# Kernel optimization log

Hardware: AMD Instinct MI355X
Metric: run time of the kernel (lower is better)

Reference implementation:

```python
import jax, jax.numpy as jnp
import numpy as np

LN_EPS = 1e-5

def silu(x):
    return x * jax.nn.sigmoid(x)

def setup_inputs() -> dict:
    key = jax.random.key(0)
    ks = jax.random.split(key, 24)
    B, D = 131072, 256
    def w(k, shape, fan_in):
        return jax.random.uniform(k, shape, jnp.float32, -1.0, 1.0) / np.sqrt(fan_in)
    inp = {
        'x': jax.random.normal(ks[0], (B, D), jnp.float32),
        # stem: Linear(D,128) -> LN(128) -> SiLU -> Linear(128,64) -> SiLU
        'stem_w1': w(ks[1], (D, 128), D), 'stem_b1': w(ks[2], (128,), D),
        'ln_g': jnp.ones((128,), jnp.float32), 'ln_b': jnp.zeros((128,), jnp.float32),
        'stem_w2': w(ks[3], (128, 64), 128), 'stem_b2': w(ks[4], (64,), 128),
        # 4 experts: Linear(64,128)->SiLU->Linear(128,64)->SiLU, stacked on axis 0
        'ew1': w(ks[5], (4, 64, 128), 64), 'eb1': w(ks[6], (4, 128), 64),
        'ew2': w(ks[7], (4, 128, 64), 128), 'eb2': w(ks[8], (4, 64), 128),
        # gate: Linear(64,32)->SiLU->Linear(32,4)
        'gw1': w(ks[9], (64, 32), 64), 'gb1': w(ks[10], (32,), 64),
        'gw2': w(ks[11], (32, 4), 32), 'gb2': w(ks[12], (4,), 32),
        # shared: Linear(64,64)->SiLU
        'sw': w(ks[13], (64, 64), 64), 'sb': w(ks[14], (64,), 64),
        # 3 heads (strain, tensile, yield) stacked: Linear(64,32)->SiLU->Linear(32,1)
        'hw1': w(ks[15], (3, 64, 32), 64), 'hb1': w(ks[16], (3, 32), 64),
        'hw2': w(ks[17], (3, 32, 1), 32), 'hb2': w(ks[18], (3, 1), 32),
    }
    return inp

def reference(x, stem_w1, stem_b1, ln_g, ln_b, stem_w2, stem_b2,
              ew1, eb1, ew2, eb2, gw1, gb1, gw2, gb2, sw, sb,
              hw1, hb1, hw2, hb2):
    # stem (dropout = identity, eval mode)
    h = x @ stem_w1 + stem_b1                      # [B,128]
    mu = jnp.mean(h, -1, keepdims=True)
    var = jnp.mean(jnp.square(h - mu), -1, keepdims=True)
    h = (h - mu) * jax.lax.rsqrt(var + LN_EPS) * ln_g + ln_b
    h = silu(h)
    h = silu(h @ stem_w2 + stem_b2)                # [B,64]
    # gate
    g = silu(h @ gw1 + gb1)
    gate_w = jax.nn.softmax(g @ gw2 + gb2, axis=-1)  # [B,4]
    # experts: [B,64] x [4,64,128] -> [B,4,128]
    e = silu(jnp.einsum('bd,edh->beh', h, ew1) + eb1)
    e = silu(jnp.einsum('beh,ehd->bed', e, ew2) + eb2)  # [B,4,64]
    moe_h = jnp.einsum('bed,be->bd', e, gate_w)    # [B,64]
    # shared trunk (dropout = identity)
    feat = silu(moe_h @ sw + sb)                   # [B,64]
    # 3 heads
    hh = silu(jnp.einsum('bd,kdh->bkh', feat, hw1) + hb1)  # [B,3,32]
    out = (jnp.einsum('bkh,kho->bko', hh, hw2) + hb2)[..., 0]  # [B,3]
    return out
```

## Files before the change

### kernel.cpp

```cpp
#include <hip/hip_runtime.h>

typedef _Float16 f16;
typedef f16   f16x4 __attribute__((ext_vector_type(4)));
typedef f16   f16x8 __attribute__((ext_vector_type(8)));
typedef float f32x4 __attribute__((ext_vector_type(4)));

#define MFMA16(a, b, c) __builtin_amdgcn_mfma_f32_16x16x32_f16((a), (b), (c), 0, 0, 0)

#define IMG_W1   0
#define IMG_W2   32768
#define IMG_GW1  40960
#define IMG_EW1  43008
#define IMG_EW2  75776
#define IMG_SW   108544
#define IMG_HW1  112640

__device__ __forceinline__ float silu_f(float v) {
    return v * __builtin_amdgcn_rcpf(1.0f + __expf(-v));
}

__device__ void conv_blk(const float* __restrict__ src, f16* __restrict__ dst,
                         int srcN, int k0, int n0, int KB, int NB, int tid, int nth) {
    for (int i = tid; i < KB * NB; i += nth) {
        const int kk = i / NB, nn = i - kk * NB;
        dst[nn * KB + (kk ^ ((nn & 7) << 3))] = (f16)src[(long)(k0 + kk) * srcN + n0 + nn];
    }
}

__global__ void prep_weights(const float* __restrict__ w1, const float* __restrict__ w2,
                             const float* __restrict__ gw1, const float* __restrict__ ew1,
                             const float* __restrict__ ew2, const float* __restrict__ sw,
                             const float* __restrict__ hw1, f16* __restrict__ ws) {
    const int tid = blockIdx.x * 256 + threadIdx.x;
    const int nth = gridDim.x * 256;
    for (int kh = 0; kh < 2; ++kh)
        for (int nh = 0; nh < 2; ++nh)
            conv_blk(w1, ws + IMG_W1 + (kh * 2 + nh) * 8192, 128, kh * 128, nh * 64, 128, 64, tid, nth);
    conv_blk(w2,  ws + IMG_W2,  64, 0, 0, 128, 64, tid, nth);
    conv_blk(gw1, ws + IMG_GW1, 32, 0, 0,  64, 32, tid, nth);
    for (int e = 0; e < 4; ++e)
        for (int h = 0; h < 2; ++h) {
            conv_blk(ew1 + e * 8192, ws + IMG_EW1 + (e * 2 + h) * 4096, 128, 0, h * 64, 64, 64, tid, nth);
            conv_blk(ew2 + e * 8192, ws + IMG_EW2 + (e * 2 + h) * 4096,  64, h * 64, 0, 64, 64, tid, nth);
        }
    conv_blk(sw, ws + IMG_SW, 64, 0, 0, 64, 64, tid, nth);
    for (int h = 0; h < 3; ++h)
        conv_blk(hw1 + h * 2048, ws + IMG_HW1 + h * 2048, 32, 0, 0, 64, 32, tid, nth);
}

#define GLL16(g, l) __builtin_amdgcn_global_load_lds(                        \
    (const __attribute__((address_space(1))) void*)(g),                     \
    (__attribute__((address_space(3))) void*)(l), 16, 0, 0)

template<int S_F16>
__device__ __forceinline__ void stage_img(const f16* __restrict__ g, f16* l,
                                          int wv, int lane) {
    constexpr int QB = (S_F16 * 2) / 4;
    constexpr int CALLS = QB / 1024;
    const char* gs = (const char*)g + wv * QB + lane * 16;
    char* ls = (char*)l + wv * QB;
    #pragma unroll
    for (int i = 0; i < CALLS; ++i)
        GLL16(gs + i * 1024, ls + i * 1024);
}

__device__ __forceinline__ int swz_key(int mode, int r) {
    if (mode == 0) return (r & 7) << 3;
    if (mode == 1) return (r & 15) << 3;
    return ((((r >> 2) & 3) << 1) | (r & 1)) << 3;
}

template<int MODE>
__device__ __forceinline__ f16x8 ld_frag(const f16* base, int stride, int row_base, int k0) {
    const int lane = threadIdx.x & 63;
    const int r = row_base + (lane & 15);
    const int k = k0 + ((lane >> 4) << 3);
    return *(const f16x8*)(base + r * stride + (k ^ swz_key(MODE, r)));
}

template<int MODE>
__device__ __forceinline__ void st_frag(f16* base, int stride, int row_base, int col_base, f32x4 v) {
    const int lane = threadIdx.x & 63;
    const int c = col_base + (lane & 15);
    #pragma unroll
    for (int g = 0; g < 4; ++g) {
        const int r = row_base + ((lane >> 4) << 2) + g;
        base[r * stride + (c ^ swz_key(MODE, r))] = (f16)v[g];
    }
}

__device__ __forceinline__ void stage_x(const float* __restrict__ xsrc, f16* XACT, int half) {
    const int t = threadIdx.x;
    #pragma unroll 8
    for (int i = 0; i < 16; ++i) {
        const int idx4 = t + i * 256;
        const int r  = idx4 >> 5;
        const int kc = (idx4 & 31) << 2;
        const float4 v = *(const float4*)(xsrc + (long)r * 256 + half * 128 + kc);
        f16x4 o; o[0] = (f16)v.x; o[1] = (f16)v.y; o[2] = (f16)v.z; o[3] = (f16)v.w;
        *(f16x4*)(XACT + r * 128 + (kc ^ ((r & 15) << 3))) = o;
    }
}

__device__ __forceinline__ f32x4 reduce16(f32x4 v) {
    #pragma unroll
    for (int m = 1; m <= 8; m <<= 1) {
        f32x4 o;
        #pragma unroll
        for (int i = 0; i < 4; ++i) o[i] = __shfl_xor(v[i], m, 64);
        v += o;
    }
    return v;
}

__global__ __launch_bounds__(256, 3)
void fused_net_mfma(const float* __restrict__ x,   const f16* __restrict__ wsp,
                    const float* __restrict__ b1,  const float* __restrict__ lng,
                    const float* __restrict__ lnb, const float* __restrict__ b2,
                    const float* __restrict__ eb1, const float* __restrict__ eb2,
                    const float* __restrict__ gb1, const float* __restrict__ gw2,
                    const float* __restrict__ gb2, const float* __restrict__ sb,
                    const float* __restrict__ hb1, const float* __restrict__ hw2,
                    const float* __restrict__ hb2, float* __restrict__ out)
{
    __shared__ __align__(16) f16 lds[26624];
    f16* XACT = lds;
    f16* ACT1 = lds;
    f16* ACT2 = lds + 8192;
    f16* W    = lds + 16384;
    f16* G    = lds + 24576;

    const int lane = threadIdx.x & 63;
    const int wv   = threadIdx.x >> 6;
    const int c    = lane & 15;
    const long blockRow = (long)blockIdx.x * 128;
    const int waveRow = wv * 32;
    const float* xblk = x + blockRow * 256;

    f32x4 acc[2][8];
    #pragma unroll
    for (int n = 0; n < 8; ++n) {
        const float bv = b1[n * 16 + c];
        f32x4 t = {bv, bv, bv, bv};
        acc[0][n] = t; acc[1][n] = t;
    }
    #pragma unroll
    for (int kh = 0; kh < 2; ++kh) {
        if (kh) __syncthreads();
        stage_x(xblk, XACT, kh);
        stage_img<8192>(wsp + IMG_W1 + kh * 16384, W, wv, lane);
        __syncthreads();
        f16x8 af[2][4];
        #pragma unroll
        for (int m = 0; m < 2; ++m)
            #pragma unroll
            for (int ks = 0; ks < 4; ++ks)
                af[m][ks] = ld_frag<1>(XACT, 128, waveRow + m * 16, ks * 32);
        #pragma unroll
        for (int ks = 0; ks < 4; ++ks)
            #pragma unroll
            for (int n = 0; n < 4; ++n) {
                const f16x8 b = ld_frag<0>(W, 128, n * 16, ks * 32);
                acc[0][n] = MFMA16(af[0][ks], b, acc[0][n]);
                acc[1][n] = MFMA16(af[1][ks], b, acc[1][n]);
            }
        __syncthreads();
        stage_img<8192>(wsp + IMG_W1 + kh * 16384 + 8192, W, wv, lane);
        __syncthreads();
        #pragma unroll
        for (int ks = 0; ks < 4; ++ks)
            #pragma unroll
            for (int n = 0; n < 4; ++n) {
                const f16x8 b = ld_frag<0>(W, 128, n * 16, ks * 32);
                acc[0][4 + n] = MFMA16(af[0][ks], b, acc[0][4 + n]);
                acc[1][4 + n] = MFMA16(af[1][ks], b, acc[1][4 + n]);
            }
    }

    f32x4 mu[2], rs[2];
    #pragma unroll
    for (int m = 0; m < 2; ++m) {
        f32x4 s = {0, 0, 0, 0}, q = {0, 0, 0, 0};
        #pragma unroll
        for (int n = 0; n < 8; ++n) { s += acc[m][n]; q += acc[m][n] * acc[m][n]; }
        s = reduce16(s); q = reduce16(q);
        mu[m] = s * 0.0078125f;
        #pragma unroll
        for (int g = 0; g < 4; ++g) {
            const float var = q[g] * 0.0078125f - mu[m][g] * mu[m][g];
            rs[m][g] = rsqrtf(var + 1e-5f);
        }
    }
    __syncthreads();
    stage_img<8192>(wsp + IMG_W2,  W, wv, lane);
    stage_img<2048>(wsp + IMG_GW1, G, wv, lane);
    __syncthreads();

    f32x4 a2[2][4];
    #pragma unroll
    for (int n = 0; n < 4; ++n) {
        const float bv = b2[n * 16 + c];
        f32x4 t = {bv, bv, bv, bv};
        a2[0][n] = t; a2[1][n] = t;
    }
    #pragma unroll
    for (int half = 0; half < 2; ++half) {
        #pragma unroll
        for (int m = 0; m < 2; ++m)
            #pragma unroll
            for (int n = 0; n < 4; ++n) {
                const int j = half * 64 + n * 16 + c;
                const float gg = lng[j], bb = lnb[j];
                f32x4 v;
                #pragma unroll
                for (int g = 0; g < 4; ++g)
                    v[g] = silu_f((acc[m][half * 4 + n][g] - mu[m][g]) * rs[m][g] * gg + bb);
                st_frag<2>(ACT1, 64, waveRow + m * 16, n * 16, v);
            }
        #pragma unroll
        for (int ks = 0; ks < 2; ++ks) {
            const f16x8 a0 = ld_frag<2>(ACT1, 64, waveRow,      ks * 32);
            const f16x8 a1 = ld_frag<2>(ACT1, 64, waveRow + 16, ks * 32);
            #pragma unroll
            for (int n = 0; n < 4; ++n) {
                const f16x8 b = ld_frag<0>(W, 128, n * 16, half * 64 + ks * 32);
                a2[0][n] = MFMA16(a0, b, a2[0][n]);
                a2[1][n] = MFMA16(a1, b, a2[1][n]);
            }
        }
    }
    #pragma unroll
    for (int m = 0; m < 2; ++m)
        #pragma unroll
        for (int n = 0; n < 4; ++n) {
            f32x4 v;
            #pragma unroll
            for (int g = 0; g < 4; ++g) v[g] = silu_f(a2[m][n][g]);
            st_frag<2>(ACT2, 64, waveRow + m * 16, n * 16, v);
        }

    f32x4 gwt[2][4];
    {
        f32x4 ag[2][2];
        #pragma unroll
        for (int n = 0; n < 2; ++n) {
            const float bv = gb1[n * 16 + c];
            f32x4 t = {bv, bv, bv, bv};
            ag[0][n] = t; ag[1][n] = t;
        }
        #pragma unroll
        for (int ks = 0; ks < 2; ++ks) {
            const f16x8 a0 = ld_frag<2>(ACT2, 64, waveRow,      ks * 32);
            const f16x8 a1 = ld_frag<2>(ACT2, 64, waveRow + 16, ks * 32);
            #pragma unroll
            for (int n = 0; n < 2; ++n) {
                const f16x8 b = ld_frag<0>(G, 64, n * 16, ks * 32);
                ag[0][n] = MFMA16(a0, b, ag[0][n]);
                ag[1][n] = MFMA16(a1, b, ag[1][n]);
            }
        }
        const f32x4 gb2v = *(const f32x4*)gb2;
        #pragma unroll
        for (int m = 0; m < 2; ++m) {
            f32x4 pg[4] = {{0,0,0,0},{0,0,0,0},{0,0,0,0},{0,0,0,0}};
            #pragma unroll
            for (int n = 0; n < 2; ++n) {
                const int j = n * 16 + c;
                const f32x4 w4 = *(const f32x4*)(gw2 + j * 4);
                #pragma unroll
                for (int g = 0; g < 4; ++g)
                    pg[g] += silu_f(ag[m][n][g]) * w4;
            }
            #pragma unroll
            for (int g = 0; g < 4; ++g) {
                f32x4 l = reduce16(pg[g]) + gb2v;
                const float mx = fmaxf(fmaxf(l[0], l[1]), fmaxf(l[2], l[3]));
                f32x4 ee;
                #pragma unroll
                for (int o = 0; o < 4; ++o) ee[o] = __expf(l[o] - mx);
                const float inv = __builtin_amdgcn_rcpf(ee[0] + ee[1] + ee[2] + ee[3]);
                gwt[m][g] = ee * inv;
            }
        }
    }

    f32x4 moe[2][4] = {{{0,0,0,0},{0,0,0,0},{0,0,0,0},{0,0,0,0}},
                       {{0,0,0,0},{0,0,0,0},{0,0,0,0},{0,0,0,0}}};
    #pragma unroll
    for (int e = 0; e < 4; ++e) {
        f32x4 a2acc[2][4];
        #pragma unroll
        for (int n = 0; n < 4; ++n) {
            const float bv = eb2[e * 64 + n * 16 + c];
            f32x4 t = {bv, bv, bv, bv};
            a2acc[0][n] = t; a2acc[1][n] = t;
        }
        #pragma unroll
        for (int mh = 0; mh < 2; ++mh) {
            __syncthreads();
            stage_img<4096>(wsp + IMG_EW1 + (e * 2 + mh) * 4096, W,        wv, lane);
            stage_img<4096>(wsp + IMG_EW2 + (e * 2 + mh) * 4096, W + 4096, wv, lane);
            __syncthreads();
            f32x4 a1acc[2][4];
            #pragma unroll
            for (int n = 0; n < 4; ++n) {
                const float bv = eb1[e * 128 + mh * 64 + n * 16 + c];
                f32x4 t = {bv, bv, bv, bv};
                a1acc[0][n] = t; a1acc[1][n] = t;
            }
            #pragma unroll
            for (int ks = 0; ks < 2; ++ks) {
                const f16x8 a0 = ld_frag<2>(ACT2, 64, waveRow,      ks * 32);
                const f16x8 a1 = ld_frag<2>(ACT2, 64, waveRow + 16, ks * 32);
                #pragma unroll
                for (int n = 0; n < 4; ++n) {
                    const f16x8 b = ld_frag<0>(W, 64, n * 16, ks * 32);
                    a1acc[0][n] = MFMA16(a0, b, a1acc[0][n]);
                    a1acc[1][n] = MFMA16(a1, b, a1acc[1][n]);
                }
            }
            #pragma unroll
            for (int m = 0; m < 2; ++m)
                #pragma unroll
                for (int n = 0; n < 4; ++n) {
                    f32x4 v;
                    #pragma unroll
                    for (int g = 0; g < 4; ++g) v[g] = silu_f(a1acc[m][n][g]);
                    st_frag<2>(ACT1, 64, waveRow + m * 16, n * 16, v);
                }
            #pragma unroll
            for (int ks = 0; ks < 2; ++ks) {
                const f16x8 a0 = ld_frag<2>(ACT1, 64, waveRow,      ks * 32);
                const f16x8 a1 = ld_frag<2>(ACT1, 64, waveRow + 16, ks * 32);
                #pragma unroll
                for (int n = 0; n < 4; ++n) {
                    const f16x8 b = ld_frag<0>(W + 4096, 64, n * 16, ks * 32);
                    a2acc[0][n] = MFMA16(a0, b, a2acc[0][n]);
                    a2acc[1][n] = MFMA16(a1, b, a2acc[1][n]);
                }
            }
        }
        #pragma unroll
        for (int m = 0; m < 2; ++m)
            #pragma unroll
            for (int n = 0; n < 4; ++n)
                #pragma unroll
                for (int g = 0; g < 4; ++g)
                    moe[m][n][g] += silu_f(a2acc[m][n][g]) * gwt[m][g][e];
    }

    #pragma unroll
    for (int m = 0; m < 2; ++m)
        #pragma unroll
        for (int n = 0; n < 4; ++n)
            st_frag<2>(ACT2, 64, waveRow + m * 16, n * 16, moe[m][n]);
    __syncthreads();
    stage_img<4096>(wsp + IMG_SW,         W,        wv, lane);
    stage_img<2048>(wsp + IMG_HW1,        W + 4096, wv, lane);
    stage_img<2048>(wsp + IMG_HW1 + 2048, W + 6144, wv, lane);
    stage_img<2048>(wsp + IMG_HW1 + 4096, G,        wv, lane);
    __syncthreads();

    {
        f32x4 as[2][4];
        #pragma unroll
        for (int n = 0; n < 4; ++n) {
            const float bv = sb[n * 16 + c];
            f32x4 t = {bv, bv, bv, bv};
            as[0][n] = t; as[1][n] = t;
        }
        #pragma unroll
        for (int ks = 0; ks < 2; ++ks) {
            const f16x8 a0 = ld_frag<2>(ACT2, 64, waveRow,      ks * 32);
            const f16x8 a1 = ld_frag<2>(ACT2, 64, waveRow + 16, ks * 32);
            #pragma unroll
            for (int n = 0; n < 4; ++n) {
                const f16x8 b = ld_frag<0>(W, 64, n * 16, ks * 32);
                as[0][n] = MFMA16(a0, b, as[0][n]);
                as[1][n] = MFMA16(a1, b, as[1][n]);
            }
        }
        #pragma unroll
        for (int m = 0; m < 2; ++m)
            #pragma unroll
            for (int n = 0; n < 4; ++n) {
                f32x4 v;
                #pragma unroll
                for (int g = 0; g < 4; ++g) v[g] = silu_f(as[m][n][g]);
                st_frag<2>(ACT1, 64, waveRow + m * 16, n * 16, v);
            }
    }

    {
        f32x4 ah[2][6];
        #pragma unroll
        for (int n = 0; n < 6; ++n) {
            const float bv = hb1[(n >> 1) * 32 + (n & 1) * 16 + c];
            f32x4 t = {bv, bv, bv, bv};
            ah[0][n] = t; ah[1][n] = t;
        }
        #pragma unroll
        for (int ks = 0; ks < 2; ++ks) {
            const f16x8 a0 = ld_frag<2>(ACT1, 64, waveRow,      ks * 32);
            const f16x8 a1 = ld_frag<2>(ACT1, 64, waveRow + 16, ks * 32);
            #pragma unroll
            for (int n = 0; n < 6; ++n) {
                const int head = n >> 1;
                const f16* hw = (head == 0) ? (W + 4096) : (head == 1) ? (W + 6144) : G;
                const f16x8 b = ld_frag<0>(hw, 64, (n & 1) * 16, ks * 32);
                ah[0][n] = MFMA16(a0, b, ah[0][n]);
                ah[1][n] = MFMA16(a1, b, ah[1][n]);
            }
        }
        const float hb2_0 = hb2[0], hb2_1 = hb2[1], hb2_2 = hb2[2];
        #pragma unroll
        for (int m = 0; m < 2; ++m) {
            f32x4 ph[3] = {{0,0,0,0},{0,0,0,0},{0,0,0,0}};
            #pragma unroll
            for (int n = 0; n < 6; ++n) {
                const int head = n >> 1;
                const int j = (n & 1) * 16 + c;
                const float w2v = hw2[head * 32 + j];
                #pragma unroll
                for (int g = 0; g < 4; ++g)
                    ph[head][g] += silu_f(ah[m][n][g]) * w2v;
            }
            #pragma unroll
            for (int h = 0; h < 3; ++h) ph[h] = reduce16(ph[h]);
            #pragma unroll
            for (int g = 0; g < 4; ++g) {
                const long row = blockRow + waveRow + m * 16 + ((lane >> 4) << 2) + g;
                if (c < 3) {
                    const float r0 = ph[0][g] + hb2_0;
                    const float r1 = ph[1][g] + hb2_1;
                    const float r2 = ph[2][g] + hb2_2;
                    out[row * 3 + c] = (c == 0) ? r0 : ((c == 1) ? r1 : r2);
                }
            }
        }
    }
}

extern "C" void kernel_launch(void* const* d_in, const int* in_sizes, int n_in,
                              void* d_out, int out_size, void* d_ws, size_t ws_size,
                              hipStream_t stream) {
    const float* x    = (const float*)d_in[0];
    const float* w1   = (const float*)d_in[1];
    const float* b1   = (const float*)d_in[2];
    const float* lng  = (const float*)d_in[3];
    const float* lnb  = (const float*)d_in[4];
    const float* w2   = (const float*)d_in[5];
    const float* b2   = (const float*)d_in[6];
    const float* ew1  = (const float*)d_in[7];
    const float* eb1  = (const float*)d_in[8];
    const float* ew2  = (const float*)d_in[9];
    const float* eb2  = (const float*)d_in[10];
    const float* gw1  = (const float*)d_in[11];
    const float* gb1  = (const float*)d_in[12];
    const float* gw2  = (const float*)d_in[13];
    const float* gb2  = (const float*)d_in[14];
    const float* sw   = (const float*)d_in[15];
    const float* sb   = (const float*)d_in[16];
    const float* hw1  = (const float*)d_in[17];
    const float* hb1  = (const float*)d_in[18];
    const float* hw2  = (const float*)d_in[19];
    const float* hb2  = (const float*)d_in[20];
    float* out = (float*)d_out;
    f16* ws = (f16*)d_ws;

    hipLaunchKernelGGL(prep_weights, dim3(64), dim3(256), 0, stream,
                       w1, w2, gw1, ew1, ew2, sw, hw1, ws);

    const int B = in_sizes[0] / 256;
    const int grid = B / 128;
    hipLaunchKernelGGL(fused_net_mfma, dim3(grid), dim3(256), 0, stream,
                       x, ws, b1, lng, lnb, b2, eb1, eb2, gb1, gw2, gb2,
                       sb, hb1, hw2, hb2, out);
}
```

Baseline: 109.1 us.

## Double-buffer weight tiles in LDS and keep per-wave activation strips

Splits all weight images into uniform 64x64 f16 tiles and stages them into two alternating LDS buffers, so the next tile's global-to-LDS load is issued while MFMAs run on the current one. Input rows are prefetched into registers one K-quarter ahead, and activations go through a small per-wave LDS strip with fragments kept in registers. This shrinks LDS from about 52KB to 37KB, which may allow more resident blocks. The aim is to hide weight-load latency behind compute and cut barrier stalls, at the cost of more complex scheduling and extra register pressure from the x prefetch.

```diff
diff --git a/kernel.cpp b/kernel.cpp
--- a/kernel.cpp
+++ b/kernel.cpp
@@ -4,6 +4,7 @@
 typedef f16   f16x4 __attribute__((ext_vector_type(4)));
 typedef f16   f16x8 __attribute__((ext_vector_type(8)));
 typedef float f32x4 __attribute__((ext_vector_type(4)));
+typedef __attribute__((address_space(3))) char as3char;
 
 #define MFMA16(a, b, c) __builtin_amdgcn_mfma_f32_16x16x32_f16((a), (b), (c), 0, 0, 0)
 
@@ -33,11 +34,12 @@
                              const float* __restrict__ hw1, f16* __restrict__ ws) {
     const int tid = blockIdx.x * 256 + threadIdx.x;
     const int nth = gridDim.x * 256;
+    for (int kq = 0; kq < 4; ++kq)
+        for (int nh = 0; nh < 2; ++nh)
+            conv_blk(w1, ws + IMG_W1 + (kq * 2 + nh) * 4096, 128, kq * 64, nh * 64, 64, 64, tid, nth);
     for (int kh = 0; kh < 2; ++kh)
-        for (int nh = 0; nh < 2; ++nh)
-            conv_blk(w1, ws + IMG_W1 + (kh * 2 + nh) * 8192, 128, kh * 128, nh * 64, 128, 64, tid, nth);
-    conv_blk(w2,  ws + IMG_W2,  64, 0, 0, 128, 64, tid, nth);
-    conv_blk(gw1, ws + IMG_GW1, 32, 0, 0,  64, 32, tid, nth);
+        conv_blk(w2, ws + IMG_W2 + kh * 4096, 64, kh * 64, 0, 64, 64, tid, nth);
+    conv_blk(gw1, ws + IMG_GW1, 32, 0, 0, 64, 32, tid, nth);
     for (int e = 0; e < 4; ++e)
         for (int h = 0; h < 2; ++h) {
             conv_blk(ew1 + e * 8192, ws + IMG_EW1 + (e * 2 + h) * 4096, 128, 0, h * 64, 64, 64, tid, nth);
@@ -48,58 +50,65 @@
         conv_blk(hw1 + h * 2048, ws + IMG_HW1 + h * 2048, 32, 0, 0, 64, 32, tid, nth);
 }
 
-#define GLL16(g, l) __builtin_amdgcn_global_load_lds(                        \
-    (const __attribute__((address_space(1))) void*)(g),                     \
-    (__attribute__((address_space(3))) void*)(l), 16, 0, 0)
-
-template<int S_F16>
-__device__ __forceinline__ void stage_img(const f16* __restrict__ g, f16* l,
-                                          int wv, int lane) {
-    constexpr int QB = (S_F16 * 2) / 4;
-    constexpr int CALLS = QB / 1024;
-    const char* gs = (const char*)g + wv * QB + lane * 16;
-    char* ls = (char*)l + wv * QB;
-    #pragma unroll
-    for (int i = 0; i < CALLS; ++i)
-        GLL16(gs + i * 1024, ls + i * 1024);
-}
-
-__device__ __forceinline__ int swz_key(int mode, int r) {
-    if (mode == 0) return (r & 7) << 3;
-    if (mode == 1) return (r & 15) << 3;
-    return ((((r >> 2) & 3) << 1) | (r & 1)) << 3;
-}
-
-template<int MODE>
-__device__ __forceinline__ f16x8 ld_frag(const f16* base, int stride, int row_base, int k0) {
-    const int lane = threadIdx.x & 63;
+template<int BYTES>
+__device__ __forceinline__ void stage4(const f16* __restrict__ g, as3char* l, int wv, int lane) {
+    constexpr int CH = BYTES / 1024;
+    #pragma unroll
+    for (int ch = 0; ch < CH; ++ch)
+        if ((ch & 3) == wv)
+            __builtin_amdgcn_global_load_lds(
+                (const __attribute__((address_space(1))) void*)((const char*)g + ch * 1024 + lane * 16),
+                (__attribute__((address_space(3))) void*)(l + ch * 1024), 16, 0, 0);
+}
+
+__device__ __forceinline__ int swzW(int n) { return (n & 7) << 3; }
+__device__ __forceinline__ int swzS(int r) { return (((((r >> 2) & 3) << 1) | (r & 1))) << 3; }
+
+__device__ __forceinline__ f16x8 ldW(const f16* base, int row_base, int k0, int lane) {
     const int r = row_base + (lane & 15);
     const int k = k0 + ((lane >> 4) << 3);
-    return *(const f16x8*)(base + r * stride + (k ^ swz_key(MODE, r)));
-}
-
-template<int MODE>
-__device__ __forceinline__ void st_frag(f16* base, int stride, int row_base, int col_base, f32x4 v) {
-    const int lane = threadIdx.x & 63;
-    const int c = col_base + (lane & 15);
+    return *(const f16x8*)(base + r * 64 + (k ^ swzW(r)));
+}
+__device__ __forceinline__ f16x8 ldS(const f16* strip, int row_base, int k0, int lane) {
+    const int r = row_base + (lane & 15);
+    const int k = k0 + ((lane >> 4) << 3);
+    return *(const f16x8*)(strip + r * 64 + (k ^ swzS(r)));
+}
+__device__ __forceinline__ void stS(f16* strip, int row_base, int col_base, f32x4 v, int lane) {
+    const int cc = col_base + (lane & 15);
     #pragma unroll
     for (int g = 0; g < 4; ++g) {
         const int r = row_base + ((lane >> 4) << 2) + g;
-        base[r * stride + (c ^ swz_key(MODE, r))] = (f16)v[g];
-    }
-}
-
-__device__ __forceinline__ void stage_x(const float* __restrict__ xsrc, f16* XACT, int half) {
-    const int t = threadIdx.x;
-    #pragma unroll 8
-    for (int i = 0; i < 16; ++i) {
-        const int idx4 = t + i * 256;
-        const int r  = idx4 >> 5;
-        const int kc = (idx4 & 31) << 2;
-        const float4 v = *(const float4*)(xsrc + (long)r * 256 + half * 128 + kc);
-        f16x4 o; o[0] = (f16)v.x; o[1] = (f16)v.y; o[2] = (f16)v.z; o[3] = (f16)v.w;
-        *(f16x4*)(XACT + r * 128 + (kc ^ ((r & 15) << 3))) = o;
-    }
+        strip[r * 64 + (cc ^ swzS(r))] = (f16)v[g];
+    }
+}
+
+__device__ __forceinline__ void mm16(const f16x8 a[2][2], const f16* wb, f32x4 acc[2][4], int lane) {
+    #pragma unroll
+    for (int ks = 0; ks < 2; ++ks)
+        #pragma unroll
+        for (int n = 0; n < 4; ++n) {
+            const f16x8 b = ldW(wb, n * 16, ks * 32, lane);
+            acc[0][n] = MFMA16(a[0][ks], b, acc[0][n]);
+            acc[1][n] = MFMA16(a[1][ks], b, acc[1][n]);
+        }
+}
+
+__device__ __forceinline__ void silu_to_frags(f16* strip, const f32x4 in[2][4], f16x8 outf[2][2], int lane) {
+    #pragma unroll
+    for (int m = 0; m < 2; ++m)
+        #pragma unroll
+        for (int n = 0; n < 4; ++n) {
+            f32x4 v;
+            #pragma unroll
+            for (int g = 0; g < 4; ++g) v[g] = silu_f(in[m][n][g]);
+            stS(strip, m * 16, n * 16, v, lane);
+        }
+    #pragma unroll
+    for (int m = 0; m < 2; ++m)
+        #pragma unroll
+        for (int ks = 0; ks < 2; ++ks)
+            outf[m][ks] = ldS(strip, m * 16, ks * 32, lane);
 }
 
 __device__ __forceinline__ f32x4 reduce16(f32x4 v) {
@@ -123,78 +132,96 @@
                     const float* __restrict__ hb1, const float* __restrict__ hw2,
                     const float* __restrict__ hb2, float* __restrict__ out)
 {
-    __shared__ __align__(16) f16 lds[26624];
-    f16* XACT = lds;
-    f16* ACT1 = lds;
-    f16* ACT2 = lds + 8192;
-    f16* W    = lds + 16384;
-    f16* G    = lds + 24576;
-
+    __shared__ __align__(16) f16 lds[18944];
+    as3char* const LB = (as3char*)lds;
     const int lane = threadIdx.x & 63;
     const int wv   = threadIdx.x >> 6;
     const int c    = lane & 15;
+    const int q    = lane >> 4;
+    f16* STRIP = lds + wv * 2048;
+    f16* const WB0 = lds + 8192;   as3char* const WB0_3 = LB + 16384;
+    f16* const WB1 = lds + 12288;  as3char* const WB1_3 = LB + 24576;
+    f16* const G   = lds + 16384;  as3char* const G_3   = LB + 32768;
+    f16* const GWT = lds + 18432;
+
     const long blockRow = (long)blockIdx.x * 128;
-    const int waveRow = wv * 32;
-    const float* xblk = x + blockRow * 256;
+    const float* xw = x + (blockRow + wv * 32) * 256;
+
+    float4 xr[8];
+    #pragma unroll
+    for (int j = 0; j < 8; ++j) {
+        const int fl = j * 64 + lane;
+        xr[j] = *(const float4*)(xw + (fl >> 4) * 256 + (fl & 15) * 4);
+    }
+    stage4<8192>(wsp + IMG_W1, WB0_3, wv, lane);
+    stage4<4096>(wsp + IMG_GW1, G_3, wv, lane);
+    __syncthreads();
 
     f32x4 acc[2][8];
     #pragma unroll
-    for (int n = 0; n < 8; ++n) {
-        const float bv = b1[n * 16 + c];
+    for (int n8 = 0; n8 < 8; ++n8) {
+        const float bv = b1[n8 * 16 + c];
         f32x4 t = {bv, bv, bv, bv};
-        acc[0][n] = t; acc[1][n] = t;
-    }
-    #pragma unroll
-    for (int kh = 0; kh < 2; ++kh) {
-        if (kh) __syncthreads();
-        stage_x(xblk, XACT, kh);
-        stage_img<8192>(wsp + IMG_W1 + kh * 16384, W, wv, lane);
-        __syncthreads();
-        f16x8 af[2][4];
-        #pragma unroll
-        for (int m = 0; m < 2; ++m)
-            #pragma unroll
-            for (int ks = 0; ks < 4; ++ks)
-                af[m][ks] = ld_frag<1>(XACT, 128, waveRow + m * 16, ks * 32);
-        #pragma unroll
-        for (int ks = 0; ks < 4; ++ks)
-            #pragma unroll
-            for (int n = 0; n < 4; ++n) {
-                const f16x8 b = ld_frag<0>(W, 128, n * 16, ks * 32);
-                acc[0][n] = MFMA16(af[0][ks], b, acc[0][n]);
-                acc[1][n] = MFMA16(af[1][ks], b, acc[1][n]);
-            }
-        __syncthreads();
-        stage_img<8192>(wsp + IMG_W1 + kh * 16384 + 8192, W, wv, lane);
-        __syncthreads();
-        #pragma unroll
-        for (int ks = 0; ks < 4; ++ks)
-            #pragma unroll
-            for (int n = 0; n < 4; ++n) {
-                const f16x8 b = ld_frag<0>(W, 128, n * 16, ks * 32);
-                acc[0][4 + n] = MFMA16(af[0][ks], b, acc[0][4 + n]);
-                acc[1][4 + n] = MFMA16(af[1][ks], b, acc[1][4 + n]);
-            }
+        acc[0][n8] = t; acc[1][n8] = t;
+    }
+
+    #pragma unroll 1
+    for (int kq = 0; kq < 4; ++kq) {
+        #pragma unroll
+        for (int j = 0; j < 8; ++j) {
+            const int fl = j * 64 + lane;
+            const int row = fl >> 4, col = (fl & 15) * 4;
+            f16x4 o; o[0] = (f16)xr[j].x; o[1] = (f16)xr[j].y; o[2] = (f16)xr[j].z; o[3] = (f16)xr[j].w;
+            *(f16x4*)(STRIP + row * 64 + (col ^ swzS(row))) = o;
+        }
+        f16x8 af[2][2];
+        #pragma unroll
+        for (int m = 0; m < 2; ++m)
+            #pragma unroll
+            for (int ks = 0; ks < 2; ++ks)
+                af[m][ks] = ldS(STRIP, m * 16, ks * 32, lane);
+
+        stage4<8192>(wsp + IMG_W1 + (kq * 2 + 1) * 4096, WB1_3, wv, lane);
+        {
+            f32x4 a4[2][4] = {{acc[0][0],acc[0][1],acc[0][2],acc[0][3]},
+                              {acc[1][0],acc[1][1],acc[1][2],acc[1][3]}};
+            mm16(af, WB0, a4, lane);
+            #pragma unroll
+            for (int n = 0; n < 4; ++n) { acc[0][n] = a4[0][n]; acc[1][n] = a4[1][n]; }
+        }
+        __syncthreads();
+
+        if (kq < 3) {
+            #pragma unroll
+            for (int j = 0; j < 8; ++j) {
+                const int fl = j * 64 + lane;
+                xr[j] = *(const float4*)(xw + (fl >> 4) * 256 + (kq + 1) * 64 + (fl & 15) * 4);
+            }
+        }
+        const f16* nsrc = (kq < 3) ? (wsp + IMG_W1 + (kq + 1) * 2 * 4096) : (wsp + IMG_W2);
+        stage4<8192>(nsrc, WB0_3, wv, lane);
+        {
+            f32x4 a4[2][4] = {{acc[0][4],acc[0][5],acc[0][6],acc[0][7]},
+                              {acc[1][4],acc[1][5],acc[1][6],acc[1][7]}};
+            mm16(af, WB1, a4, lane);
+            #pragma unroll
+            for (int n = 0; n < 4; ++n) { acc[0][4 + n] = a4[0][n]; acc[1][4 + n] = a4[1][n]; }
+        }
+        __syncthreads();
     }
 
     f32x4 mu[2], rs[2];
     #pragma unroll
     for (int m = 0; m < 2; ++m) {
-        f32x4 s = {0, 0, 0, 0}, q = {0, 0, 0, 0};
-        #pragma unroll
-        for (int n = 0; n < 8; ++n) { s += acc[m][n]; q += acc[m][n] * acc[m][n]; }
-        s = reduce16(s); q = reduce16(q);
+        f32x4 s = {0,0,0,0}, qq = {0,0,0,0};
+        #pragma unroll
+        for (int n8 = 0; n8 < 8; ++n8) { s += acc[m][n8]; qq += acc[m][n8] * acc[m][n8]; }
+        s = reduce16(s); qq = reduce16(qq);
         mu[m] = s * 0.0078125f;
         #pragma unroll
-        for (int g = 0; g < 4; ++g) {
-            const float var = q[g] * 0.0078125f - mu[m][g] * mu[m][g];
-            rs[m][g] = rsqrtf(var + 1e-5f);
-        }
-    }
-    __syncthreads();
-    stage_img<8192>(wsp + IMG_W2,  W, wv, lane);
-    stage_img<2048>(wsp + IMG_GW1, G, wv, lane);
-    __syncthreads();
+        for (int g = 0; g < 4; ++g)
+            rs[m][g] = rsqrtf(qq[g] * 0.0078125f - mu[m][g] * mu[m][g] + 1e-5f);
+    }
 
     f32x4 a2[2][4];
     #pragma unroll
@@ -203,193 +230,158 @@
         f32x4 t = {bv, bv, bv, bv};
         a2[0][n] = t; a2[1][n] = t;
     }
-    #pragma unroll
-    for (int half = 0; half < 2; ++half) {
+    f16x8 hbA[2][2];
+
+    #pragma unroll 1
+    for (int kh = 0; kh < 2; ++kh) {
+        if (kh == 0) stage4<8192>(wsp + IMG_W2 + 4096, WB1_3, wv, lane);
+        else         stage4<8192>(wsp + IMG_EW1, WB0_3, wv, lane);
         #pragma unroll
         for (int m = 0; m < 2; ++m)
             #pragma unroll
             for (int n = 0; n < 4; ++n) {
-                const int j = half * 64 + n * 16 + c;
+                const int j = kh * 64 + n * 16 + c;
                 const float gg = lng[j], bb = lnb[j];
                 f32x4 v;
                 #pragma unroll
                 for (int g = 0; g < 4; ++g)
-                    v[g] = silu_f((acc[m][half * 4 + n][g] - mu[m][g]) * rs[m][g] * gg + bb);
-                st_frag<2>(ACT1, 64, waveRow + m * 16, n * 16, v);
-            }
-        #pragma unroll
-        for (int ks = 0; ks < 2; ++ks) {
-            const f16x8 a0 = ld_frag<2>(ACT1, 64, waveRow,      ks * 32);
-            const f16x8 a1 = ld_frag<2>(ACT1, 64, waveRow + 16, ks * 32);
-            #pragma unroll
-            for (int n = 0; n < 4; ++n) {
-                const f16x8 b = ld_frag<0>(W, 128, n * 16, half * 64 + ks * 32);
-                a2[0][n] = MFMA16(a0, b, a2[0][n]);
-                a2[1][n] = MFMA16(a1, b, a2[1][n]);
-            }
-        }
-    }
-    #pragma unroll
-    for (int m = 0; m < 2; ++m)
-        #pragma unroll
-        for (int n = 0; n < 4; ++n) {
-            f32x4 v;
-            #pragma unroll
-            for (int g = 0; g < 4; ++g) v[g] = silu_f(a2[m][n][g]);
-            st_frag<2>(ACT2, 64, waveRow + m * 16, n * 16, v);
-        }
-
-    f32x4 gwt[2][4];
-    {
-        f32x4 ag[2][2];
-        #pragma unroll
-        for (int n = 0; n < 2; ++n) {
-            const float bv = gb1[n * 16 + c];
-            f32x4 t = {bv, bv, bv, bv};
-            ag[0][n] = t; ag[1][n] = t;
-        }
-        #pragma unroll
-        for (int ks = 0; ks < 2; ++ks) {
-            const f16x8 a0 = ld_frag<2>(ACT2, 64, waveRow,      ks * 32);
-            const f16x8 a1 = ld_frag<2>(ACT2, 64, waveRow + 16, ks * 32);
+                    v[g] = silu_f((acc[m][kh * 4 + n][g] - mu[m][g]) * rs[m][g] * gg + bb);
+                stS(STRIP, m * 16, n * 16, v, lane);
+            }
+        f16x8 af[2][2];
+        #pragma unroll
+        for (int m = 0; m < 2; ++m)
+            #pragma unroll
+            for (int ks = 0; ks < 2; ++ks)
+                af[m][ks] = ldS(STRIP, m * 16, ks * 32, lane);
+        mm16(af, kh == 0 ? WB0 : WB1, a2, lane);
+        if (kh == 1) {
+            silu_to_frags(STRIP, a2, hbA, lane);
+            f32x4 ag[2][2];
             #pragma unroll
             for (int n = 0; n < 2; ++n) {
-                const f16x8 b = ld_frag<0>(G, 64, n * 16, ks * 32);
-                ag[0][n] = MFMA16(a0, b, ag[0][n]);
-                ag[1][n] = MFMA16(a1, b, ag[1][n]);
-            }
-        }
-        const f32x4 gb2v = *(const f32x4*)gb2;
-        #pragma unroll
-        for (int m = 0; m < 2; ++m) {
-            f32x4 pg[4] = {{0,0,0,0},{0,0,0,0},{0,0,0,0},{0,0,0,0}};
-            #pragma unroll
-            for (int n = 0; n < 2; ++n) {
-                const int j = n * 16 + c;
-                const f32x4 w4 = *(const f32x4*)(gw2 + j * 4);
-                #pragma unroll
-                for (int g = 0; g < 4; ++g)
-                    pg[g] += silu_f(ag[m][n][g]) * w4;
-            }
-            #pragma unroll
-            for (int g = 0; g < 4; ++g) {
-                f32x4 l = reduce16(pg[g]) + gb2v;
-                const float mx = fmaxf(fmaxf(l[0], l[1]), fmaxf(l[2], l[3]));
-                f32x4 ee;
-                #pragma unroll
-                for (int o = 0; o < 4; ++o) ee[o] = __expf(l[o] - mx);
-                const float inv = __builtin_amdgcn_rcpf(ee[0] + ee[1] + ee[2] + ee[3]);
-                gwt[m][g] = ee * inv;
-            }
-        }
+                const float bv = gb1[n * 16 + c];
+                f32x4 t = {bv, bv, bv, bv};
+                ag[0][n] = t; ag[1][n] = t;
+            }
+            #pragma unroll
+            for (int ks = 0; ks < 2; ++ks)
+                #pragma unroll
+                for (int n = 0; n < 2; ++n) {
+                    const f16x8 b = ldW(G, n * 16, ks * 32, lane);
+                    ag[0][n] = MFMA16(hbA[0][ks], b, ag[0][n]);
+                    ag[1][n] = MFMA16(hbA[1][ks], b, ag[1][n]);
+                }
+            const f32x4 gb2v = *(const f32x4*)gb2;
+            #pragma unroll
+            for (int m = 0; m < 2; ++m) {
+                f32x4 pg[4] = {{0,0,0,0},{0,0,0,0},{0,0,0,0},{0,0,0,0}};
+                #pragma unroll
+                for (int n = 0; n < 2; ++n) {
+                    const f32x4 w4 = *(const f32x4*)(gw2 + (n * 16 + c) * 4);
+                    #pragma unroll
+                    for (int g = 0; g < 4; ++g)
+                        pg[g] += silu_f(ag[m][n][g]) * w4;
+                }
+                #pragma unroll
+                for (int g = 0; g < 4; ++g) {
+                    f32x4 l = reduce16(pg[g]) + gb2v;
+                    const float mx = fmaxf(fmaxf(l[0], l[1]), fmaxf(l[2], l[3]));
+                    f32x4 ee;
+                    #pragma unroll
+                    for (int o = 0; o < 4; ++o) ee[o] = __expf(l[o] - mx);
+                    const f32x4 gv = ee * __builtin_amdgcn_rcpf(ee[0] + ee[1] + ee[2] + ee[3]);
+                    if (c < 4) {
+                        const float val = (c == 0) ? gv[0] : (c == 1) ? gv[1] : (c == 2) ? gv[2] : gv[3];
+                        GWT[wv * 128 + c * 32 + m * 16 + q * 4 + g] = (f16)val;
+                    }
+                }
+            }
+        }
+        __syncthreads();
     }
 
     f32x4 moe[2][4] = {{{0,0,0,0},{0,0,0,0},{0,0,0,0},{0,0,0,0}},
                        {{0,0,0,0},{0,0,0,0},{0,0,0,0},{0,0,0,0}}};
-    #pragma unroll
+    #pragma unroll 1
     for (int e = 0; e < 4; ++e) {
-        f32x4 a2acc[2][4];
+        f16x8 ea[2][2];
+        f32x4 a2e[2][4];
         #pragma unroll
         for (int n = 0; n < 4; ++n) {
             const float bv = eb2[e * 64 + n * 16 + c];
             f32x4 t = {bv, bv, bv, bv};
-            a2acc[0][n] = t; a2acc[1][n] = t;
-        }
-        #pragma unroll
-        for (int mh = 0; mh < 2; ++mh) {
-            __syncthreads();
-            stage_img<4096>(wsp + IMG_EW1 + (e * 2 + mh) * 4096, W,        wv, lane);
-            stage_img<4096>(wsp + IMG_EW2 + (e * 2 + mh) * 4096, W + 4096, wv, lane);
-            __syncthreads();
-            f32x4 a1acc[2][4];
+            a2e[0][n] = t; a2e[1][n] = t;
+        }
+        stage4<8192>(wsp + IMG_EW2 + (e * 2) * 4096, WB1_3, wv, lane);
+        {
+            f32x4 aa[2][4];
             #pragma unroll
             for (int n = 0; n < 4; ++n) {
-                const float bv = eb1[e * 128 + mh * 64 + n * 16 + c];
+                const float bv = eb1[e * 128 + n * 16 + c];
                 f32x4 t = {bv, bv, bv, bv};
-                a1acc[0][n] = t; a1acc[1][n] = t;
-            }
-            #pragma unroll
-            for (int ks = 0; ks < 2; ++ks) {
-                const f16x8 a0 = ld_frag<2>(ACT2, 64, waveRow,      ks * 32);
-                const f16x8 a1 = ld_frag<2>(ACT2, 64, waveRow + 16, ks * 32);
-                #pragma unroll
-                for (int n = 0; n < 4; ++n) {
-                    const f16x8 b = ld_frag<0>(W, 64, n * 16, ks * 32);
-                    a1acc[0][n] = MFMA16(a0, b, a1acc[0][n]);
-                    a1acc[1][n] = MFMA16(a1, b, a1acc[1][n]);
-                }
-            }
-            #pragma unroll
-            for (int m = 0; m < 2; ++m)
-                #pragma unroll
-                for (int n = 0; n < 4; ++n) {
-                    f32x4 v;
-                    #pragma unroll
-                    for (int g = 0; g < 4; ++g) v[g] = silu_f(a1acc[m][n][g]);
-                    st_frag<2>(ACT1, 64, waveRow + m * 16, n * 16, v);
-                }
-            #pragma unroll
-            for (int ks = 0; ks < 2; ++ks) {
-                const f16x8 a0 = ld_frag<2>(ACT1, 64, waveRow,      ks * 32);
-                const f16x8 a1 = ld_frag<2>(ACT1, 64, waveRow + 16, ks * 32);
-                #pragma unroll
-                for (int n = 0; n < 4; ++n) {
-                    const f16x8 b = ld_frag<0>(W + 4096, 64, n * 16, ks * 32);
-                    a2acc[0][n] = MFMA16(a0, b, a2acc[0][n]);
-                    a2acc[1][n] = MFMA16(a1, b, a2acc[1][n]);
-                }
-            }
-        }
+                aa[0][n] = t; aa[1][n] = t;
+            }
+            mm16(hbA, WB0, aa, lane);
+            silu_to_frags(STRIP, aa, ea, lane);
+        }
+        __syncthreads();
+        stage4<8192>(wsp + IMG_EW1 + (e * 2 + 1) * 4096, WB0_3, wv, lane);
+        mm16(ea, WB1, a2e, lane);
+        __syncthreads();
+        stage4<8192>(wsp + IMG_EW2 + (e * 2 + 1) * 4096, WB1_3, wv, lane);
+        {
+            f32x4 aa[2][4];
+            #pragma unroll
+            for (int n = 0; n < 4; ++n) {
+                const float bv = eb1[e * 128 + 64 + n * 16 + c];
+                f32x4 t = {bv, bv, bv, bv};
+                aa[0][n] = t; aa[1][n] = t;
+            }
+            mm16(hbA, WB0, aa, lane);
+            silu_to_frags(STRIP, aa, ea, lane);
+        }
+        __syncthreads();
+        stage4<8192>((e < 3) ? (wsp + IMG_EW1 + (e + 1) * 2 * 4096) : (wsp + IMG_SW), WB0_3, wv, lane);
+        mm16(ea, WB1, a2e, lane);
+        #pragma unroll
+        for (int m = 0; m < 2; ++m)
+            #pragma unroll
+            for (int g = 0; g < 4; ++g) {
+                const float ge = (float)GWT[wv * 128 + e * 32 + m * 16 + q * 4 + g];
+                #pragma unroll
+                for (int n = 0; n < 4; ++n)
+                    moe[m][n][g] += silu_f(a2e[m][n][g]) * ge;
+            }
+        __syncthreads();
+    }
+
+    stage4<8192>(wsp + IMG_HW1, WB1_3, wv, lane);
+    stage4<4096>(wsp + IMG_HW1 + 4096, G_3, wv, lane);
+    f16x8 featA[2][2];
+    {
         #pragma unroll
         for (int m = 0; m < 2; ++m)
             #pragma unroll
             for (int n = 0; n < 4; ++n)
-                #pragma unroll
-                for (int g = 0; g < 4; ++g)
-                    moe[m][n][g] += silu_f(a2acc[m][n][g]) * gwt[m][g][e];
-    }
-
-    #pragma unroll
-    for (int m = 0; m < 2; ++m)
-        #pragma unroll
-        for (int n = 0; n < 4; ++n)
-            st_frag<2>(ACT2, 64, waveRow + m * 16, n * 16, moe[m][n]);
-    __syncthreads();
-    stage_img<4096>(wsp + IMG_SW,         W,        wv, lane);
-    stage_img<2048>(wsp + IMG_HW1,        W + 4096, wv, lane);
-    stage_img<2048>(wsp + IMG_HW1 + 2048, W + 6144, wv, lane);
-    stage_img<2048>(wsp + IMG_HW1 + 4096, G,        wv, lane);
-    __syncthreads();
-
-    {
-        f32x4 as[2][4];
+                stS(STRIP, m * 16, n * 16, moe[m][n], lane);
+        f16x8 ma[2][2];
+        #pragma unroll
+        for (int m = 0; m < 2; ++m)
+            #pragma unroll
+            for (int ks = 0; ks < 2; ++ks)
+                ma[m][ks] = ldS(STRIP, m * 16, ks * 32, lane);
+        f32x4 fs[2][4];
         #pragma unroll
         for (int n = 0; n < 4; ++n) {
             const float bv = sb[n * 16 + c];
             f32x4 t = {bv, bv, bv, bv};
-            as[0][n] = t; as[1][n] = t;
-        }
-        #pragma unroll
-        for (int ks = 0; ks < 2; ++ks) {
-            const f16x8 a0 = ld_frag<2>(ACT2, 64, waveRow,      ks * 32);
-            const f16x8 a1 = ld_frag<2>(ACT2, 64, waveRow + 16, ks * 32);
-            #pragma unroll
-            for (int n = 0; n < 4; ++n) {
-                const f16x8 b = ld_frag<0>(W, 64, n * 16, ks * 32);
-                as[0][n] = MFMA16(a0, b, as[0][n]);
-                as[1][n] = MFMA16(a1, b, as[1][n]);
-            }
-        }
-        #pragma unroll
-        for (int m = 0; m < 2; ++m)
-            #pragma unroll
-            for (int n = 0; n < 4; ++n) {
-                f32x4 v;
-                #pragma unroll
-                for (int g = 0; g < 4; ++g) v[g] = silu_f(as[m][n][g]);
-                st_frag<2>(ACT1, 64, waveRow + m * 16, n * 16, v);
-            }
-    }
+            fs[0][n] = t; fs[1][n] = t;
+        }
+        mm16(ma, WB0, fs, lane);
+        silu_to_frags(STRIP, fs, featA, lane);
+    }
+    __syncthreads();
 
     {
         f32x4 ah[2][6];
@@ -400,36 +392,32 @@
             ah[0][n] = t; ah[1][n] = t;
         }
         #pragma unroll
-        for (int ks = 0; ks < 2; ++ks) {
-            const f16x8 a0 = ld_frag<2>(ACT1, 64, waveRow,      ks * 32);
-            const f16x8 a1 = ld_frag<2>(ACT1, 64, waveRow + 16, ks * 32);
+        for (int ks = 0; ks < 2; ++ks)
             #pragma unroll
             for (int n = 0; n < 6; ++n) {
-                const int head = n >> 1;
-                const f16* hw = (head == 0) ? (W + 4096) : (head == 1) ? (W + 6144) : G;
-                const f16x8 b = ld_frag<0>(hw, 64, (n & 1) * 16, ks * 32);
-                ah[0][n] = MFMA16(a0, b, ah[0][n]);
-                ah[1][n] = MFMA16(a1, b, ah[1][n]);
-            }
-        }
+                const int h = n >> 1;
+                const f16* hw = (h < 2) ? (WB1 + h * 2048) : G;
+                const f16x8 b = ldW(hw, (n & 1) * 16, ks * 32, lane);
+                ah[0][n] = MFMA16(featA[0][ks], b, ah[0][n]);
+                ah[1][n] = MFMA16(featA[1][ks], b, ah[1][n]);
+            }
         const float hb2_0 = hb2[0], hb2_1 = hb2[1], hb2_2 = hb2[2];
         #pragma unroll
         for (int m = 0; m < 2; ++m) {
             f32x4 ph[3] = {{0,0,0,0},{0,0,0,0},{0,0,0,0}};
             #pragma unroll
             for (int n = 0; n < 6; ++n) {
-                const int head = n >> 1;
-                const int j = (n & 1) * 16 + c;
-                const float w2v = hw2[head * 32 + j];
+                const int h = n >> 1;
+                const float w2v = hw2[h * 32 + (n & 1) * 16 + c];
                 #pragma unroll
                 for (int g = 0; g < 4; ++g)
-                    ph[head][g] += silu_f(ah[m][n][g]) * w2v;
+                    ph[h][g] += silu_f(ah[m][n][g]) * w2v;
             }
             #pragma unroll
             for (int h = 0; h < 3; ++h) ph[h] = reduce16(ph[h]);
             #pragma unroll
             for (int g = 0; g < 4; ++g) {
-                const long row = blockRow + waveRow + m * 16 + ((lane >> 4) << 2) + g;
+                const long row = blockRow + wv * 32 + m * 16 + q * 4 + g;
                 if (c < 3) {
                     const float r0 = ph[0][g] + hb2_0;
                     const float r1 = ph[1][g] + hb2_1;
```

Measured after the change: 160.1 us. +46.7%, slower.
